# Kernel optimization log

Hardware: AMD Instinct MI355X
Metric: run time of the kernel (lower is better)

## Reference

```python
import jax, jax.numpy as jnp
import numpy as np

B, L, V, D, H, DK, NL, M = 4, 1024, 64, 256, 4, 64, 4, 20
FF = 4 * D
EPS = 1e-5


def _rel_table(seq_len, m):
    # abs(i-j), log-bucketed beyond m, clipped to [0, 2m] -> int indices [L, L]
    d = jnp.abs(jnp.arange(seq_len)[:, None] - jnp.arange(seq_len)[None, :]).astype(jnp.float32)
    d = jnp.where(d > m, m + jnp.log2(jnp.maximum(d - m, 1.0)), d)
    return jnp.clip(d, 0, 2 * m).astype(jnp.int32)


def _layer_norm(x, g, b):
    mu = jnp.mean(x, axis=-1, keepdims=True)
    var = jnp.mean(jnp.square(x - mu), axis=-1, keepdims=True)
    return (x - mu) * jax.lax.rsqrt(var + EPS) * g + b


def setup_inputs() -> dict:
    key = jax.random.key(0)
    ks = jax.random.split(key, 16)
    w = lambda i, shape: jax.random.normal(ks[i], shape, jnp.float32) * 0.05
    return {
        "x": jax.random.normal(ks[0], (B, L, V), jnp.float32),
        "emb": w(1, (V, D)),
        "Wq": w(2, (NL, D, H * DK)), "bq": jnp.zeros((NL, H * DK), jnp.float32),
        "Wk": w(3, (NL, D, H * DK)), "bk": jnp.zeros((NL, H * DK), jnp.float32),
        "Wv": w(4, (NL, D, H * DK)), "bv": jnp.zeros((NL, H * DK), jnp.float32),
        "Wo": w(5, (NL, H * DK, D)), "bo": jnp.zeros((NL, D), jnp.float32),
        "rel_k": 1.0 + w(6, (NL, 2 * M + 1, H)),  # multiplicative bias ~1
        "rel_b": w(7, (NL, 2 * M + 1, H)),
        "ln1_g": jnp.ones((NL, D), jnp.float32), "ln1_b": jnp.zeros((NL, D), jnp.float32),
        "W1": w(8, (NL, D, FF)), "b1": jnp.zeros((NL, FF), jnp.float32),
        "W2": w(9, (NL, FF, D)), "b2": jnp.zeros((NL, D), jnp.float32),
        "ln2_g": jnp.ones((NL, D), jnp.float32), "ln2_b": jnp.zeros((NL, D), jnp.float32),
    }


def reference(x, emb, Wq, bq, Wk, bk, Wv, bv, Wo, bo, rel_k, rel_b,
              ln1_g, ln1_b, W1, b1, W2, b2, ln2_g, ln2_b):
    h = x @ emb  # [B, L, D]  (dropout inactive: eval mode)
    table = _rel_table(L, M)  # [L, L] int32
    inv_sqrt_dk = jnp.float32(1.0 / np.sqrt(DK))
    attns = []
    for l in range(NL):
        q = (h @ Wq[l] + bq[l]).reshape(B, L, H, DK)
        k = (h @ Wk[l] + bk[l]).reshape(B, L, H, DK)
        v = (h @ Wv[l] + bv[l]).reshape(B, L, H, DK)
        scores = jnp.einsum('blhk,bmhk->bhlm', q, k) * inv_sqrt_dk
        # per-head relative-position bias (table symmetric, so axis order of L,L is immaterial)
        bias_k = jnp.transpose(rel_k[l][table], (2, 1, 0))  # [H, L, L]
        bias_b = jnp.transpose(rel_b[l][table], (2, 1, 0))  # [H, L, L]
        scores = scores * bias_k[None] + bias_b[None]
        attn = jax.nn.softmax(scores, axis=-1)  # attn dropout inactive (eval)
        attns.append(attn)
        out = jnp.einsum('bhlm,bmhk->blhk', attn, v).reshape(B, L, H * DK) @ Wo[l] + bo[l]
        # FeedForwardNetwork (note: source has NO residual connections)
        y = _layer_norm(out, ln1_g[l], ln1_b[l])
        y = jax.nn.gelu(y @ W1[l] + b1[l], approximate=False) @ W2[l] + b2[l]
        h = _layer_norm(y, ln2_g[l], ln2_b[l])
    avg_attn = jnp.mean(jnp.stack(attns, axis=0), axis=0)  # [B, H, L, L]
    return h.mean(axis=1), avg_attn
```

## Files before the change

kernel.cpp:

```cpp
#include <hip/hip_runtime.h>
#include <hip/hip_bf16.h>
#include <math.h>

#define Bn 4
#define Ln 1024
#define Vn 64
#define Dn 256
#define Hn 4
#define DKn 64
#define NLn 4
#define Mn 20
#define FFn 1024
#define NTOK (Bn * Ln)
#define QKVW 768
#define LOG2E 1.4426950408889634f
#define PELEMS (Bn * Hn * Ln * Ln)

typedef __attribute__((ext_vector_type(8))) short bf16x8;
typedef __attribute__((ext_vector_type(4))) float f32x4;

__device__ __forceinline__ ushort f2b(float f) {
    uint u = __float_as_uint(f);
    u += 0x7fff + ((u >> 16) & 1);
    return (ushort)(u >> 16);
}
__device__ __forceinline__ float b2f(ushort u) {
    return __uint_as_float(((uint)u) << 16);
}

__global__ __launch_bounds__(256) void embed_k(const float* __restrict__ X,
                                               const float* __restrict__ E,
                                               ushort* __restrict__ Hb) {
    __shared__ float xs[Vn];
    int n = blockIdx.x, d = threadIdx.x;
    if (threadIdx.x < Vn) xs[threadIdx.x] = X[n * Vn + threadIdx.x];
    __syncthreads();
    float s = 0.f;
#pragma unroll
    for (int v = 0; v < Vn; ++v) s += xs[v] * E[v * Dn + d];
    Hb[(size_t)n * Dn + d] = f2b(s);
}

__global__ __launch_bounds__(256) void relbias_k(const float* __restrict__ rk,
                                                 const float* __restrict__ rb,
                                                 float* __restrict__ bkT,
                                                 float* __restrict__ bbT) {
    int tid = blockIdx.x * 256 + threadIdx.x;
    int dist = tid & 1023;
    int hh = (tid >> 10) & 3;
    int l = tid >> 12;
    float dd = (float)dist;
    if (dist > Mn) dd = (float)Mn + log2f((float)(dist - Mn));
    if (dd > 2.0f * Mn) dd = 2.0f * Mn;
    int idx = (int)dd;
    bkT[tid] = rk[(l * (2 * Mn + 1) + idx) * Hn + hh] * 0.125f * LOG2E;
    bbT[tid] = rb[(l * (2 * Mn + 1) + idx) * Hn + hh] * LOG2E;
}

__global__ __launch_bounds__(256) void prep_bias(const float* __restrict__ bq,
                                                 const float* __restrict__ bk,
                                                 const float* __restrict__ bv,
                                                 float* __restrict__ bqkv) {
    int idx = blockIdx.x * 256 + threadIdx.x;
    int l = idx / QKVW, r = idx - l * QKVW;
    float v;
    if (r < 256)      v = bq[l * 256 + r];
    else if (r < 512) v = bk[l * 256 + r - 256];
    else              v = bv[l * 256 + r - 512];
    bqkv[idx] = v;
}

__global__ __launch_bounds__(256) void transpose_cvt(
    const float* __restrict__ src, ushort* __restrict__ dst,
    int R, int C, int srcLS, int dstLS) {
    __shared__ float s[32][33];
    src += (size_t)blockIdx.z * srcLS;
    dst += (size_t)blockIdx.z * dstLS;
    int r0 = blockIdx.y * 32, c0 = blockIdx.x * 32;
    int tx = threadIdx.x & 31, ty = threadIdx.x >> 5;
#pragma unroll
    for (int ii = 0; ii < 4; ++ii)
        s[ty + 8 * ii][tx] = src[(size_t)(r0 + ty + 8 * ii) * C + c0 + tx];
    __syncthreads();
#pragma unroll
    for (int ii = 0; ii < 4; ++ii)
        dst[(size_t)(c0 + ty + 8 * ii) * R + r0 + tx] = f2b(s[tx][ty + 8 * ii]);
}

#define GST 40
#define GEMM_FRAG_MFMA                                                        \
    bf16x8 a0 = *(const bf16x8*)&As[(wm * 32 + l15) * GST + lg * 8];          \
    bf16x8 a1 = *(const bf16x8*)&As[(wm * 32 + 16 + l15) * GST + lg * 8];     \
    bf16x8 b0 = *(const bf16x8*)&Bs[(wn * 32 + l15) * GST + lg * 8];          \
    bf16x8 b1 = *(const bf16x8*)&Bs[(wn * 32 + 16 + l15) * GST + lg * 8];     \
    acc[0][0] = __builtin_amdgcn_mfma_f32_16x16x32_bf16(a0, b0, acc[0][0], 0, 0, 0); \
    acc[0][1] = __builtin_amdgcn_mfma_f32_16x16x32_bf16(a0, b1, acc[0][1], 0, 0, 0); \
    acc[1][0] = __builtin_amdgcn_mfma_f32_16x16x32_bf16(a1, b0, acc[1][0], 0, 0, 0); \
    acc[1][1] = __builtin_amdgcn_mfma_f32_16x16x32_bf16(a1, b1, acc[1][1], 0, 0, 0);

template <int LNA>
__global__ __launch_bounds__(256) void gemm_mfma(
    const ushort* __restrict__ A, const ushort* __restrict__ Bt,
    const float* __restrict__ bias, ushort* __restrict__ C,
    int M, int N, int K, int act,
    const float* __restrict__ lng, const float* __restrict__ lnb,
    ushort* __restrict__ Vt_out) {
    __shared__ __align__(16) ushort As[64 * GST];
    __shared__ __align__(16) ushort Bs[64 * GST];
    __shared__ float gl[256];
    __shared__ float bl[256];
    int t = threadIdx.x;
    int lane = t & 63, w = t >> 6;
    int wm = w >> 1, wn = w & 1;
    int l15 = lane & 15, lg = lane >> 4;
    int mBase = blockIdx.y * 64, nBase = blockIdx.x * 64;
    int lrow = t >> 2, lkc = (t & 3) * 8;
    const ushort* Ap = A + (size_t)(mBase + lrow) * K + lkc;
    const ushort* Bp = Bt + (size_t)(nBase + lrow) * K + lkc;
    f32x4 acc[2][2] = {};

    if constexpr (LNA) {
        uint4 areg[8];
        float s = 0.f;
#pragma unroll
        for (int kc = 0; kc < 8; ++kc) {
            areg[kc] = *(const uint4*)(Ap + kc * 32);
            const ushort* e = (const ushort*)&areg[kc];
#pragma unroll
            for (int q = 0; q < 8; ++q) s += b2f(e[q]);
        }
        s += __shfl_xor(s, 1, 64);
        s += __shfl_xor(s, 2, 64);
        float mu = s * (1.0f / 256.0f);
        float vv = 0.f;
#pragma unroll
        for (int kc = 0; kc < 8; ++kc) {
            const ushort* e = (const ushort*)&areg[kc];
#pragma unroll
            for (int q = 0; q < 8; ++q) {
                float d = b2f(e[q]) - mu;
                vv += d * d;
            }
        }
        vv += __shfl_xor(vv, 1, 64);
        vv += __shfl_xor(vv, 2, 64);
        float rs = rsqrtf(vv * (1.0f / 256.0f) + 1e-5f);
        gl[t] = lng[t];
        bl[t] = lnb[t];
        __syncthreads();
#pragma unroll
        for (int kc = 0; kc < 8; ++kc) {
            uint4 bv = *(const uint4*)(Bp + kc * 32);
            __syncthreads();
            {
                const ushort* e = (const ushort*)&areg[kc];
                ushort outv[8];
#pragma unroll
                for (int q = 0; q < 8; ++q) {
                    int col = kc * 32 + lkc + q;
                    outv[q] = f2b((b2f(e[q]) - mu) * rs * gl[col] + bl[col]);
                }
                *(uint4*)&As[lrow * GST + lkc] = *(const uint4*)outv;
            }
            *(uint4*)&Bs[lrow * GST + lkc] = bv;
            __syncthreads();
            GEMM_FRAG_MFMA
        }
    } else {
        for (int k0 = 0; k0 < K; k0 += 32) {
            uint4 av = *(const uint4*)(Ap + k0);
            uint4 bv = *(const uint4*)(Bp + k0);
            __syncthreads();
            *(uint4*)&As[lrow * GST + lkc] = av;
            *(uint4*)&Bs[lrow * GST + lkc] = bv;
            __syncthreads();
            GEMM_FRAG_MFMA
        }
    }
    if (Vt_out != nullptr && nBase >= 512) {
#pragma unroll
        for (int ni = 0; ni < 2; ++ni) {
            int col = nBase + wn * 32 + ni * 16 + l15;
            float bc = bias[col];
            int d = col - 512;
#pragma unroll
            for (int mi = 0; mi < 2; ++mi) {
                int rb = mBase + wm * 32 + mi * 16 + lg * 4;
                int bb_ = rb >> 10, i_ = rb & 1023;
                size_t vb = ((size_t)(bb_ * 4 + (d >> 6)) * 64 + (d & 63)) * Ln + i_;
                ushort o4[4];
#pragma unroll
                for (int j = 0; j < 4; ++j) o4[j] = f2b(acc[mi][ni][j] + bc);
                *(ushort4*)&Vt_out[vb] = *(const ushort4*)o4;
            }
        }
        return;
    }
#pragma unroll
    for (int ni = 0; ni < 2; ++ni) {
        int col = nBase + wn * 32 + ni * 16 + l15;
        float bc = bias[col];
#pragma unroll
        for (int mi = 0; mi < 2; ++mi) {
            int rb = mBase + wm * 32 + mi * 16 + lg * 4;
#pragma unroll
            for (int j = 0; j < 4; ++j) {
                float v = acc[mi][ni][j] + bc;
                if (act) v = v * 0.5f * (1.0f + erff(v * 0.7071067811865475f));
                C[(size_t)(rb + j) * N + col] = f2b(v);
            }
        }
    }
}

#define PWST 40
#define NW 8
template <int MODE>
__global__ __launch_bounds__(512) void attn_fused(
    const ushort* __restrict__ qkv, const ushort* __restrict__ Vt,
    const float* __restrict__ bkTab, const float* __restrict__ bbTab,
    ushort* __restrict__ ctx, float* __restrict__ avg,
    ushort* __restrict__ Pout, int first) {
    __shared__ float bk_l[Ln];
    __shared__ float bb_l[Ln];
    __shared__ __align__(16) char uni[20480];
    __shared__ float mm[NW][16];
    __shared__ float ll[NW][16];

    int t = threadIdx.x;
    int lane = t & 63, w = t >> 6;
    int wn = w & 3, wc = w >> 2;
    int l15 = lane & 15, lg = lane >> 4;

    ushort* pwh = (ushort*)&uni[w * 2560];
    ushort* pwl = (ushort*)&uni[w * 2560 + 1280];

    int bid = blockIdx.x;
    int xcd = bid & 7, sub = bid >> 3;
    int bh = xcd * 2 + (sub >> 6);
    int q = sub & 63;
    int b = bh >> 2, hh = bh & 3;
    int i0 = q * 16;

#pragma unroll
    for (int ii = 0; ii < 2; ++ii) {
        bk_l[t + 512 * ii] = bkTab[hh * Ln + t + 512 * ii];
        bb_l[t + 512 * ii] = bbTab[hh * Ln + t + 512 * ii];
    }
    __syncthreads();

    bf16x8 qa0, qa1;
    {
        const ushort* qp = qkv + (size_t)(b * Ln + i0 + l15) * QKVW + hh * DKn;
        qa0 = *(const bf16x8*)(qp + lg * 8);
        qa1 = *(const bf16x8*)(qp + 32 + lg * 8);
    }

    const ushort* kbase = qkv + (size_t)(b * Ln) * QKVW + Dn + hh * DKn;

    f32x4 sv[8];
    float m[4] = {-1e30f, -1e30f, -1e30f, -1e30f};
#pragma unroll
    for (int cl = 0; cl < 8; ++cl) {
        int c = wc * 8 + cl;
        const ushort* kp = kbase + (size_t)(c * 64 + wn * 16 + l15) * QKVW;
        bf16x8 k0 = *(const bf16x8*)(kp + lg * 8);
        bf16x8 k1 = *(const bf16x8*)(kp + 32 + lg * 8);
        f32x4 acc = {};
        acc = __builtin_amdgcn_mfma_f32_16x16x32_bf16(qa0, k0, acc, 0, 0, 0);
        acc = __builtin_amdgcn_mfma_f32_16x16x32_bf16(qa1, k1, acc, 0, 0, 0);
        int j = c * 64 + wn * 16 + l15;
#pragma unroll
        for (int r = 0; r < 4; ++r) {
            int i = i0 + lg * 4 + r;
            int dist = (i > j) ? (i - j) : (j - i);
            float s = acc[r] * bk_l[dist] + bb_l[dist];
            sv[cl][r] = s;
            m[r] = fmaxf(m[r], s);
        }
    }
#pragma unroll
    for (int mask = 1; mask < 16; mask <<= 1)
#pragma unroll
        for (int r = 0; r < 4; ++r) m[r] = fmaxf(m[r], __shfl_xor(m[r], mask, 64));
    if (l15 == 0)
#pragma unroll
        for (int r = 0; r < 4; ++r) mm[w][lg * 4 + r] = m[r];
    __syncthreads();
#pragma unroll
    for (int r = 0; r < 4; ++r) {
        int row = lg * 4 + r;
        float m0 = fmaxf(fmaxf(mm[0][row], mm[1][row]), fmaxf(mm[2][row], mm[3][row]));
        float m1 = fmaxf(fmaxf(mm[4][row], mm[5][row]), fmaxf(mm[6][row], mm[7][row]));
        m[r] = fmaxf(m0, m1);
    }
    float lsum[4] = {0.f, 0.f, 0.f, 0.f};
#pragma unroll
    for (int cl = 0; cl < 8; ++cl)
#pragma unroll
        for (int r = 0; r < 4; ++r) {
            float p = exp2f(sv[cl][r] - m[r]);
            sv[cl][r] = p;
            lsum[r] += p;
        }
#pragma unroll
    for (int mask = 1; mask < 16; mask <<= 1)
#pragma unroll
        for (int r = 0; r < 4; ++r) lsum[r] += __shfl_xor(lsum[r], mask, 64);
    if (l15 == 0)
#pragma unroll
        for (int r = 0; r < 4; ++r) ll[w][lg * 4 + r] = lsum[r];
    __syncthreads();
    float invl[4];
#pragma unroll
    for (int r = 0; r < 4; ++r) {
        int row = lg * 4 + r;
        invl[r] = 1.0f / (ll[0][row] + ll[1][row] + ll[2][row] + ll[3][row] +
                          ll[4][row] + ll[5][row] + ll[6][row] + ll[7][row]);
    }

    const ushort* vbase = Vt + (size_t)bh * DKn * Ln;
    float* avgrow = avg + ((size_t)bh * Ln + i0) * Ln;
    ushort* prow = Pout + ((size_t)bh * Ln + i0) * Ln;
    int iw = lane >> 2, jq = lane & 3;
    f32x4 acco[4] = {};
#pragma unroll
    for (int p = 0; p < 4; ++p) {
        const int c0 = wc * 8 + 2 * p, c1 = c0 + 1;
        float aold[2][4];
        if (MODE == 0 && !first) {
#pragma unroll
            for (int cc = 0; cc < 2; ++cc)
#pragma unroll
                for (int r = 0; r < 4; ++r)
                    aold[cc][r] = avgrow[(size_t)(lg * 4 + r) * Ln +
                                         (c0 + cc) * 64 + wn * 16 + l15];
        }
#pragma unroll
        for (int cc = 0; cc < 2; ++cc)
#pragma unroll
            for (int r = 0; r < 4; ++r) {
                float pv = sv[2 * p + cc][r] * invl[r];
                sv[2 * p + cc][r] = pv;
                ushort ph = f2b(pv);
                int off = (lg * 4 + r) * PWST + cc * 16 + l15;
                pwh[off] = ph;
                pwl[off] = f2b(pv - b2f(ph));
            }
        int kcol = (lg < 2 ? c0 : c1) * 64 + wn * 16 + (lg & 1) * 8;
        bf16x8 va0 = *(const bf16x8*)(vbase + (size_t)(0 * 16 + l15) * Ln + kcol);
        bf16x8 va1 = *(const bf16x8*)(vbase + (size_t)(1 * 16 + l15) * Ln + kcol);
        bf16x8 va2 = *(const bf16x8*)(vbase + (size_t)(2 * 16 + l15) * Ln + kcol);
        bf16x8 va3 = *(const bf16x8*)(vbase + (size_t)(3 * 16 + l15) * Ln + kcol);
        bf16x8 pbh = *(const bf16x8*)&pwh[l15 * PWST + lg * 8];
        bf16x8 pbl = *(const bf16x8*)&pwl[l15 * PWST + lg * 8];
        acco[0] = __builtin_amdgcn_mfma_f32_16x16x32_bf16(va0, pbh, acco[0], 0, 0, 0);
        acco[1] = __builtin_amdgcn_mfma_f32_16x16x32_bf16(va1, pbh, acco[1], 0, 0, 0);
        acco[2] = __builtin_amdgcn_mfma_f32_16x16x32_bf16(va2, pbh, acco[2], 0, 0, 0);
        acco[3] = __builtin_amdgcn_mfma_f32_16x16x32_bf16(va3, pbh, acco[3], 0, 0, 0);
        acco[0] = __builtin_amdgcn_mfma_f32_16x16x32_bf16(va0, pbl, acco[0], 0, 0, 0);
        acco[1] = __builtin_amdgcn_mfma_f32_16x16x32_bf16(va1, pbl, acco[1], 0, 0, 0);
        acco[2] = __builtin_amdgcn_mfma_f32_16x16x32_bf16(va2, pbl, acco[2], 0, 0, 0);
        acco[3] = __builtin_amdgcn_mfma_f32_16x16x32_bf16(va3, pbl, acco[3], 0, 0, 0);
        if (MODE == 0) {
#pragma unroll
            for (int cc = 0; cc < 2; ++cc)
#pragma unroll
                for (int r = 0; r < 4; ++r) {
                    float v = 0.25f * sv[2 * p + cc][r];
                    if (!first) v += aold[cc][r];
                    avgrow[(size_t)(lg * 4 + r) * Ln + (c0 + cc) * 64 + wn * 16 + l15] = v;
                }
        } else if (MODE == 1) {
            ushort4 ph0 = *(const ushort4*)&pwh[iw * PWST + 0 * 16 + jq * 4];
            ushort4 ph1 = *(const ushort4*)&pwh[iw * PWST + 1 * 16 + jq * 4];
            *(ushort4*)&prow[(size_t)iw * Ln + c0 * 64 + wn * 16 + jq * 4] = ph0;
            *(ushort4*)&prow[(size_t)iw * Ln + c1 * 64 + wn * 16 + jq * 4] = ph1;
        } else {
#pragma unroll
            for (int cc = 0; cc < 2; ++cc) {
                int c = c0 + cc;
                size_t base = ((size_t)(bh * Ln) + i0 + iw) * Ln +
                              c * 64 + wn * 16 + jq * 4;
                ushort4 p0 = *(const ushort4*)&Pout[base];
                ushort4 p1 = *(const ushort4*)&Pout[(size_t)PELEMS + base];
                ushort4 p2 = *(const ushort4*)&Pout[(size_t)2 * PELEMS + base];
                ushort4 p3 = *(const ushort4*)&pwh[iw * PWST + cc * 16 + jq * 4];
                const ushort* q0 = (const ushort*)&p0;
                const ushort* q1 = (const ushort*)&p1;
                const ushort* q2 = (const ushort*)&p2;
                const ushort* q3 = (const ushort*)&p3;
                float4 o;
                float* op_ = (float*)&o;
#pragma unroll
                for (int k = 0; k < 4; ++k)
                    op_[k] = 0.25f * (b2f(q0[k]) + b2f(q1[k]) + b2f(q2[k]) + b2f(q3[k]));
                *(float4*)&avg[base] = o;
            }
        }
    }

    __syncthreads();
    {
        float* op = (float*)&uni[wn * 4096];
        if (wc == 1) {
#pragma unroll
            for (int dg = 0; dg < 4; ++dg)
#pragma unroll
                for (int r = 0; r < 4; ++r)
                    op[(dg * 16 + lg * 4 + r) * 16 + l15] = acco[dg][r];
        }
    }
    __syncthreads();
    {
        float* op = (float*)&uni[wn * 4096];
        if (wc == 0) {
#pragma unroll
            for (int dg = 0; dg < 4; ++dg)
#pragma unroll
                for (int r = 0; r < 4; ++r)
                    op[(dg * 16 + lg * 4 + r) * 16 + l15] += acco[dg][r];
        }
    }
    __syncthreads();
#pragma unroll
    for (int k = 0; k < 2; ++k) {
        int idx = t + 512 * k;
        float v = ((const float*)&uni[0])[idx] + ((const float*)&uni[4096])[idx] +
                  ((const float*)&uni[8192])[idx] + ((const float*)&uni[12288])[idx];
        int dd = idx >> 4, ii = idx & 15;
        ctx[(size_t)(b * Ln + i0 + ii) * Dn + hh * DKn + dd] = f2b(v);
    }
}

__global__ __launch_bounds__(256) void layernorm_k(const ushort* __restrict__ X,
                                                   const float* __restrict__ g,
                                                   const float* __restrict__ bta,
                                                   ushort* __restrict__ Y) {
    int w = threadIdx.x >> 6, lane = threadIdx.x & 63;
    int row = blockIdx.x * 4 + w;
    const ushort* xr = X + (size_t)row * Dn;
    float x[4];
#pragma unroll
    for (int ii = 0; ii < 4; ++ii) x[ii] = b2f(xr[lane + 64 * ii]);
    float s = x[0] + x[1] + x[2] + x[3];
#pragma unroll
    for (int m = 1; m < 64; m <<= 1) s += __shfl_xor(s, m, 64);
    float mu = s * (1.0f / 256.0f);
    float vs = 0.f;
#pragma unroll
    for (int ii = 0; ii < 4; ++ii) {
        float d = x[ii] - mu;
        vs += d * d;
    }
#pragma unroll
    for (int m = 1; m < 64; m <<= 1) vs += __shfl_xor(vs, m, 64);
    float rs = rsqrtf(vs * (1.0f / 256.0f) + 1e-5f);
#pragma unroll
    for (int ii = 0; ii < 4; ++ii) {
        int d = lane + 64 * ii;
        Y[(size_t)row * Dn + d] = f2b((x[ii] - mu) * rs * g[d] + bta[d]);
    }
}

__global__ __launch_bounds__(256) void mean_part_k(const ushort* __restrict__ Hb,
                                                   float* __restrict__ part) {
    int blk = blockIdx.x;
    int b = blk >> 4, g = blk & 15;
    int d = threadIdx.x;
    float s = 0.f;
#pragma unroll
    for (int r = 0; r < 64; ++r)
        s += b2f(Hb[(size_t)(b * Ln + g * 64 + r) * Dn + d]);
    part[(size_t)blk * Dn + d] = s;
}
__global__ __launch_bounds__(256) void mean_final_k(const float* __restrict__ part,
                                                    float* __restrict__ out) {
    int b = blockIdx.x, d = threadIdx.x;
    float s = 0.f;
#pragma unroll
    for (int g = 0; g < 16; ++g) s += part[(size_t)(b * 16 + g) * Dn + d];
    out[b * Dn + d] = s * (1.0f / (float)Ln);
}

extern "C" void kernel_launch(void* const* d_in, const int* in_sizes, int n_in,
                              void* d_out, int out_size, void* d_ws, size_t ws_size,
                              hipStream_t stream) {
    const float* x    = (const float*)d_in[0];
    const float* emb  = (const float*)d_in[1];
    const float* Wq   = (const float*)d_in[2];
    const float* bq   = (const float*)d_in[3];
    const float* Wk   = (const float*)d_in[4];
    const float* bk   = (const float*)d_in[5];
    const float* Wv   = (const float*)d_in[6];
    const float* bv   = (const float*)d_in[7];
    const float* Wo   = (const float*)d_in[8];
    const float* bo   = (const float*)d_in[9];
    const float* rk   = (const float*)d_in[10];
    const float* rb   = (const float*)d_in[11];
    const float* ln1g = (const float*)d_in[12];
    const float* ln1b = (const float*)d_in[13];
    const float* W1   = (const float*)d_in[14];
    const float* b1   = (const float*)d_in[15];
    const float* W2   = (const float*)d_in[16];
    const float* b2   = (const float*)d_in[17];
    const float* ln2g = (const float*)d_in[18];
    const float* ln2b = (const float*)d_in[19];

    float* out = (float*)d_out;
    float* avg = out + Bn * Dn;

    char* ws = (char*)d_ws;
    const size_t MB = 1024 * 1024;
    ushort* hb   = (ushort*)(ws);
    ushort* qkvb = (ushort*)(ws + 2 * MB);
    ushort* ctxb = (ushort*)(ws + 8 * MB);
    ushort* t1   = (ushort*)(ws + 10 * MB);
    ushort* ffb  = (ushort*)(ws + 12 * MB);
    ushort* qkvT = (ushort*)(ws + 20 * MB);
    ushort* WoT  = (ushort*)(ws + 22 * MB);
    ushort* W1T  = (ushort*)(ws + 23 * MB);
    ushort* W2T  = (ushort*)(ws + 25 * MB);
    float*  bqkv = (float*)(ws + 27 * MB);
    float*  bkT  = (float*)(ws + 27 * MB + 65536);
    float*  bbT  = (float*)(ws + 27 * MB + 131072);
    ushort* Vt   = (ushort*)(ws + 30 * MB);
    float*  mpart= (float*)(ws + 33 * MB);
    ushort* Pbuf = (ushort*)(ws + 36 * MB);

    const size_t need = 36 * MB + (size_t)3 * PELEMS * sizeof(ushort);
    const bool fancy = (ws_size >= need);

    embed_k<<<NTOK, 256, 0, stream>>>(x, emb, hb);
    relbias_k<<<64, 256, 0, stream>>>(rk, rb, bkT, bbT);
    prep_bias<<<12, 256, 0, stream>>>(bq, bk, bv, bqkv);

    dim3 t88(8, 8, NLn);
    transpose_cvt<<<t88, 256, 0, stream>>>(Wq, qkvT + 0,      256, 256, 65536, 196608);
    transpose_cvt<<<t88, 256, 0, stream>>>(Wk, qkvT + 65536,  256, 256, 65536, 196608);
    transpose_cvt<<<t88, 256, 0, stream>>>(Wv, qkvT + 131072, 256, 256, 65536, 196608);
    transpose_cvt<<<t88, 256, 0, stream>>>(Wo, WoT,           256, 256, 65536, 65536);
    transpose_cvt<<<dim3(32, 8, NLn), 256, 0, stream>>>(W1, W1T, 256, 1024, 262144, 262144);
    transpose_cvt<<<dim3(8, 32, NLn), 256, 0, stream>>>(W2, W2T, 1024, 256, 262144, 262144);

    for (int l = 0; l < NLn; ++l) {
        if (l == 0) {
            gemm_mfma<0><<<dim3(12, 64), 256, 0, stream>>>(
                hb, qkvT + (size_t)l * 196608, bqkv + l * QKVW, qkvb,
                NTOK, QKVW, Dn, 0, nullptr, nullptr, Vt);
        } else {
            gemm_mfma<1><<<dim3(12, 64), 256, 0, stream>>>(
                hb, qkvT + (size_t)l * 196608, bqkv + l * QKVW, qkvb,
                NTOK, QKVW, Dn, 0, ln2g + (l - 1) * 256, ln2b + (l - 1) * 256, Vt);
        }
        if (fancy) {
            if (l < 3) {
                attn_fused<1><<<1024, 512, 0, stream>>>(
                    qkvb, Vt, bkT + l * Hn * Ln, bbT + l * Hn * Ln, ctxb, avg,
                    Pbuf + (size_t)l * PELEMS, 0);
            } else {
                attn_fused<2><<<1024, 512, 0, stream>>>(
                    qkvb, Vt, bkT + l * Hn * Ln, bbT + l * Hn * Ln, ctxb, avg,
                    Pbuf, 0);
            }
        } else {
            attn_fused<0><<<1024, 512, 0, stream>>>(
                qkvb, Vt, bkT + l * Hn * Ln, bbT + l * Hn * Ln, ctxb, avg,
                (ushort*)Pbuf, (l == 0) ? 1 : 0);
        }
        gemm_mfma<0><<<dim3(4, 64), 256, 0, stream>>>(
            ctxb, WoT + (size_t)l * 65536, bo + l * 256, t1,
            NTOK, Dn, Dn, 0, nullptr, nullptr, nullptr);
        gemm_mfma<1><<<dim3(16, 64), 256, 0, stream>>>(
            t1, W1T + (size_t)l * 262144, b1 + l * FFn, ffb,
            NTOK, FFn, Dn, 1, ln1g + l * 256, ln1b + l * 256, nullptr);
        gemm_mfma<0><<<dim3(4, 64), 256, 0, stream>>>(
            ffb, W2T + (size_t)l * 262144, b2 + l * 256, hb,
            NTOK, Dn, FFn, 0, nullptr, nullptr, nullptr);
    }
    layernorm_k<<<NTOK / 4, 256, 0, stream>>>(
        hb, ln2g + 3 * 256, ln2b + 3 * 256, hb);
    mean_part_k<<<64, 256, 0, stream>>>(hb, mpart);
    mean_final_k<<<Bn, 256, 0, stream>>>(mpart, out);
}
```

Baseline: 391.8 us.

## Double GEMM K-tile to 64 and store attention probabilities in thread-linear order

New measurement: 375.5 us, median of 2. 1.04x faster.

```diff
diff --git a/kernel.cpp b/kernel.cpp
--- a/kernel.cpp
+++ b/kernel.cpp
@@ -87,16 +87,18 @@
         dst[(size_t)(c0 + ty + 8 * ii) * R + r0 + tx] = f2b(s[tx][ty + 8 * ii]);
 }
 
-#define GST 40
-#define GEMM_FRAG_MFMA                                                        \
-    bf16x8 a0 = *(const bf16x8*)&As[(wm * 32 + l15) * GST + lg * 8];          \
-    bf16x8 a1 = *(const bf16x8*)&As[(wm * 32 + 16 + l15) * GST + lg * 8];     \
-    bf16x8 b0 = *(const bf16x8*)&Bs[(wn * 32 + l15) * GST + lg * 8];          \
-    bf16x8 b1 = *(const bf16x8*)&Bs[(wn * 32 + 16 + l15) * GST + lg * 8];     \
-    acc[0][0] = __builtin_amdgcn_mfma_f32_16x16x32_bf16(a0, b0, acc[0][0], 0, 0, 0); \
-    acc[0][1] = __builtin_amdgcn_mfma_f32_16x16x32_bf16(a0, b1, acc[0][1], 0, 0, 0); \
-    acc[1][0] = __builtin_amdgcn_mfma_f32_16x16x32_bf16(a1, b0, acc[1][0], 0, 0, 0); \
-    acc[1][1] = __builtin_amdgcn_mfma_f32_16x16x32_bf16(a1, b1, acc[1][1], 0, 0, 0);
+#define GST 72
+#define GEMM_KK_MFMA(KK)                                                      \
+    {                                                                         \
+        bf16x8 a0 = *(const bf16x8*)&As[(wm * 32 + l15) * GST + (KK)*32 + lg * 8];      \
+        bf16x8 a1 = *(const bf16x8*)&As[(wm * 32 + 16 + l15) * GST + (KK)*32 + lg * 8]; \
+        bf16x8 b0 = *(const bf16x8*)&Bs[(wn * 32 + l15) * GST + (KK)*32 + lg * 8];      \
+        bf16x8 b1 = *(const bf16x8*)&Bs[(wn * 32 + 16 + l15) * GST + (KK)*32 + lg * 8]; \
+        acc[0][0] = __builtin_amdgcn_mfma_f32_16x16x32_bf16(a0, b0, acc[0][0], 0, 0, 0); \
+        acc[0][1] = __builtin_amdgcn_mfma_f32_16x16x32_bf16(a0, b1, acc[0][1], 0, 0, 0); \
+        acc[1][0] = __builtin_amdgcn_mfma_f32_16x16x32_bf16(a1, b0, acc[1][0], 0, 0, 0); \
+        acc[1][1] = __builtin_amdgcn_mfma_f32_16x16x32_bf16(a1, b1, acc[1][1], 0, 0, 0); \
+    }
 
 template <int LNA>
 __global__ __launch_bounds__(256) void gemm_mfma(
@@ -114,7 +116,7 @@
     int wm = w >> 1, wn = w & 1;
     int l15 = lane & 15, lg = lane >> 4;
     int mBase = blockIdx.y * 64, nBase = blockIdx.x * 64;
-    int lrow = t >> 2, lkc = (t & 3) * 8;
+    int lrow = t >> 2, lkc = (t & 3) * 16;
     const ushort* Ap = A + (size_t)(mBase + lrow) * K + lkc;
     const ushort* Bp = Bt + (size_t)(nBase + lrow) * K + lkc;
     f32x4 acc[2][2] = {};
@@ -123,12 +125,14 @@
         uint4 areg[8];
         float s = 0.f;
 #pragma unroll
-        for (int kc = 0; kc < 8; ++kc) {
-            areg[kc] = *(const uint4*)(Ap + kc * 32);
-            const ushort* e = (const ushort*)&areg[kc];
-#pragma unroll
-            for (int q = 0; q < 8; ++q) s += b2f(e[q]);
-        }
+        for (int kc = 0; kc < 4; ++kc)
+#pragma unroll
+            for (int h = 0; h < 2; ++h) {
+                areg[kc * 2 + h] = *(const uint4*)(Ap + kc * 64 + h * 8);
+                const ushort* e = (const ushort*)&areg[kc * 2 + h];
+#pragma unroll
+                for (int q = 0; q < 8; ++q) s += b2f(e[q]);
+            }
         s += __shfl_xor(s, 1, 64);
         s += __shfl_xor(s, 2, 64);
         float mu = s * (1.0f / 256.0f);
@@ -149,32 +153,41 @@
         bl[t] = lnb[t];
         __syncthreads();
 #pragma unroll
-        for (int kc = 0; kc < 8; ++kc) {
-            uint4 bv = *(const uint4*)(Bp + kc * 32);
+        for (int kc = 0; kc < 4; ++kc) {
+            uint4 bv0 = *(const uint4*)(Bp + kc * 64);
+            uint4 bv1 = *(const uint4*)(Bp + kc * 64 + 8);
             __syncthreads();
-            {
-                const ushort* e = (const ushort*)&areg[kc];
+#pragma unroll
+            for (int h = 0; h < 2; ++h) {
+                const ushort* e = (const ushort*)&areg[kc * 2 + h];
                 ushort outv[8];
 #pragma unroll
                 for (int q = 0; q < 8; ++q) {
-                    int col = kc * 32 + lkc + q;
+                    int col = kc * 64 + lkc + h * 8 + q;
                     outv[q] = f2b((b2f(e[q]) - mu) * rs * gl[col] + bl[col]);
                 }
-                *(uint4*)&As[lrow * GST + lkc] = *(const uint4*)outv;
-            }
-            *(uint4*)&Bs[lrow * GST + lkc] = bv;
+                *(uint4*)&As[lrow * GST + lkc + h * 8] = *(const uint4*)outv;
+            }
+            *(uint4*)&Bs[lrow * GST + lkc] = bv0;
+            *(uint4*)&Bs[lrow * GST + lkc + 8] = bv1;
             __syncthreads();
-            GEMM_FRAG_MFMA
+            GEMM_KK_MFMA(0)
+            GEMM_KK_MFMA(1)
         }
     } else {
-        for (int k0 = 0; k0 < K; k0 += 32) {
-            uint4 av = *(const uint4*)(Ap + k0);
-            uint4 bv = *(const uint4*)(Bp + k0);
+        for (int k0 = 0; k0 < K; k0 += 64) {
+            uint4 av0 = *(const uint4*)(Ap + k0);
+            uint4 av1 = *(const uint4*)(Ap + k0 + 8);
+            uint4 bv0 = *(const uint4*)(Bp + k0);
+            uint4 bv1 = *(const uint4*)(Bp + k0 + 8);
             __syncthreads();
-            *(uint4*)&As[lrow * GST + lkc] = av;
-            *(uint4*)&Bs[lrow * GST + lkc] = bv;
+            *(uint4*)&As[lrow * GST + lkc] = av0;
+            *(uint4*)&As[lrow * GST + lkc + 8] = av1;
+            *(uint4*)&Bs[lrow * GST + lkc] = bv0;
+            *(uint4*)&Bs[lrow * GST + lkc + 8] = bv1;
             __syncthreads();
-            GEMM_FRAG_MFMA
+            GEMM_KK_MFMA(0)
+            GEMM_KK_MFMA(1)
         }
     }
     if (Vt_out != nullptr && nBase >= 512) {
@@ -321,7 +334,6 @@
 
     const ushort* vbase = Vt + (size_t)bh * DKn * Ln;
     float* avgrow = avg + ((size_t)bh * Ln + i0) * Ln;
-    ushort* prow = Pout + ((size_t)bh * Ln + i0) * Ln;
     int iw = lane >> 2, jq = lane & 3;
     f32x4 acco[4] = {};
 #pragma unroll
@@ -372,24 +384,27 @@
                     avgrow[(size_t)(lg * 4 + r) * Ln + (c0 + cc) * 64 + wn * 16 + l15] = v;
                 }
         } else if (MODE == 1) {
+            size_t tb = ((((size_t)bid * 8 + w) * 4 + p) * 2) * 256 + (size_t)lane * 4;
             ushort4 ph0 = *(const ushort4*)&pwh[iw * PWST + 0 * 16 + jq * 4];
             ushort4 ph1 = *(const ushort4*)&pwh[iw * PWST + 1 * 16 + jq * 4];
-            *(ushort4*)&prow[(size_t)iw * Ln + c0 * 64 + wn * 16 + jq * 4] = ph0;
-            *(ushort4*)&prow[(size_t)iw * Ln + c1 * 64 + wn * 16 + jq * 4] = ph1;
+            *(ushort4*)&Pout[tb] = ph0;
+            *(ushort4*)&Pout[tb + 256] = ph1;
         } else {
 #pragma unroll
             for (int cc = 0; cc < 2; ++cc) {
                 int c = c0 + cc;
-                size_t base = ((size_t)(bh * Ln) + i0 + iw) * Ln +
-                              c * 64 + wn * 16 + jq * 4;
-                ushort4 p0 = *(const ushort4*)&Pout[base];
-                ushort4 p1 = *(const ushort4*)&Pout[(size_t)PELEMS + base];
-                ushort4 p2 = *(const ushort4*)&Pout[(size_t)2 * PELEMS + base];
+                size_t tb = ((((size_t)bid * 8 + w) * 4 + p) * 2 + cc) * 256 +
+                            (size_t)lane * 4;
+                ushort4 p0 = *(const ushort4*)&Pout[tb];
+                ushort4 p1 = *(const ushort4*)&Pout[(size_t)PELEMS + tb];
+                ushort4 p2 = *(const ushort4*)&Pout[(size_t)2 * PELEMS + tb];
                 ushort4 p3 = *(const ushort4*)&pwh[iw * PWST + cc * 16 + jq * 4];
                 const ushort* q0 = (const ushort*)&p0;
                 const ushort* q1 = (const ushort*)&p1;
                 const ushort* q2 = (const ushort*)&p2;
                 const ushort* q3 = (const ushort*)&p3;
+                size_t base = ((size_t)(bh * Ln) + i0 + iw) * Ln +
+                              c * 64 + wn * 16 + jq * 4;
                 float4 o;
                 float* op_ = (float*)&o;
 #pragma unroll
```
